# Performance work log

Measured on AMD Instinct MI355X. Metric: run time of the kernel, lower is better.

## Reference

```python
import jax, jax.numpy as jnp
import numpy as np
import math

D_PAIR = 64
N_HEADS = 4
D_HEAD = D_PAIR // N_HEADS


def setup_inputs() -> dict:
    key = jax.random.key(0)
    ks = jax.random.split(key, 9)
    B, L, D = 2, 256, D_PAIR
    s = 1.0 / math.sqrt(D)
    return {
        "z": jax.random.normal(ks[0], (B, L, L, D), dtype=jnp.float32),
        "ln_scale": jnp.ones((D,), jnp.float32),
        "ln_bias": jnp.zeros((D,), jnp.float32),
        "Wq": jax.random.normal(ks[1], (D, D), jnp.float32) * s,
        "Wk": jax.random.normal(ks[2], (D, D), jnp.float32) * s,
        "Wv": jax.random.normal(ks[3], (D, D), jnp.float32) * s,
        "Wg": jax.random.normal(ks[4], (D, D), jnp.float32) * s,
        "bg": jax.random.normal(ks[5], (D,), jnp.float32) * 0.02,
        "Wo": jax.random.normal(ks[6], (D, D), jnp.float32) * s,
        "bo": jax.random.normal(ks[7], (D,), jnp.float32) * 0.02,
    }


def _layernorm(x, scale, bias, eps=1e-5):
    mu = jnp.mean(x, axis=-1, keepdims=True)
    var = jnp.var(x, axis=-1, keepdims=True)
    return (x - mu) * jax.lax.rsqrt(var + eps) * scale + bias


def reference(z, ln_scale, ln_bias, Wq, Wk, Wv, Wg, bg, Wo, bo):
    B, L, _, D = z.shape
    H, Dh = N_HEADS, D_HEAD
    zn = _layernorm(z, ln_scale, ln_bias)
    # torch Linear(no bias): x @ W.T
    Q = (zn @ Wq.T).reshape(B, L, L, H, Dh)
    K = (zn @ Wk.T).reshape(B, L, L, H, Dh)
    V = (zn @ Wv.T).reshape(B, L, L, H, Dh)
    scale = 1.0 / math.sqrt(Dh)
    # row-wise attention: for each row l, attend over column index j
    attn = jnp.einsum("blihd,bljhd->blhij", Q, K) * scale  # [B,L,H,L,L]
    attn = jax.nn.softmax(attn, axis=-1)
    out = jnp.einsum("blhij,bljhd->blihd", attn, V).reshape(B, L, L, D)
    gate = jax.nn.sigmoid(zn @ Wg.T + bg)
    out = gate * out
    return out @ Wo.T + bo
```

## Files before the change

kernel.cpp:

```cpp
#include <hip/hip_runtime.h>
#include <hip/hip_bf16.h>
#include <math.h>


typedef __attribute__((ext_vector_type(4))) float f32x4;
typedef __attribute__((ext_vector_type(8))) short s16x8;

#define MFMA16(a, b, c) __builtin_amdgcn_mfma_f32_16x16x32_bf16((a), (b), (c), 0, 0, 0)

__device__ __forceinline__ float exp2a(float x) {
    float r;
    asm("v_exp_f32 %0, %1" : "=v"(r) : "v"(x));
    return r;
}
__device__ __forceinline__ float rcpa(float x) {
    float r;
    asm("v_rcp_f32 %0, %1" : "=v"(r) : "v"(x));
    return r;
}

__device__ __forceinline__ unsigned pk2(float a, float b) {
    union { __hip_bfloat162 h; unsigned u; } c;
    float2 t; t.x = a; t.y = b;
    c.h = __float22bfloat162_rn(t);
    return c.u;
}
__device__ __forceinline__ s16x8 cvt8(const float* p) {
    union { unsigned u[4]; s16x8 v; } r;
    r.u[0] = pk2(p[0], p[1]); r.u[1] = pk2(p[2], p[3]);
    r.u[2] = pk2(p[4], p[5]); r.u[3] = pk2(p[6], p[7]);
    return r.v;
}

static constexpr int WSLICE = 2560;
static constexpr int ZNL = 0;
static constexpr int KSH = 10240;
static constexpr int VT  = 14336;
static constexpr int LDS_EL = 18560;

__global__ __launch_bounds__(256, 3)
void ka_fused(const float* __restrict__ z, const float* __restrict__ ln_s,
              const float* __restrict__ ln_b, const float* __restrict__ Wq,
              const float* __restrict__ Wk, const float* __restrict__ Wv,
              const float* __restrict__ Wg, const float* __restrict__ bg,
              short* __restrict__ ws)
{
    __shared__ __align__(16) short lds[LDS_EL];
    const int tid = threadIdx.x, lane = tid & 63, w = tid >> 6;
    const int n16 = lane & 15, quad = lane >> 4;
    const bool qlo = (quad < 2);
    const int g = blockIdx.x, bl = g >> 2, h = g & 3;
    const size_t rowbase = (size_t)bl * (256 * 64);
    const int wsl = w * WSLICE;

    union { unsigned u[32]; s16x8 v8[8]; } row;
    {
        float zn[64];
        const float4* zp4 = (const float4*)(z + rowbase + (size_t)tid * 64);
        #pragma unroll
        for (int gq = 0; gq < 16; ++gq) {
            float4 v4 = zp4[gq];
            zn[gq * 4 + 0] = v4.x; zn[gq * 4 + 1] = v4.y;
            zn[gq * 4 + 2] = v4.z; zn[gq * 4 + 3] = v4.w;
        }
        float mu = 0.f;
        #pragma unroll
        for (int k = 0; k < 64; ++k) mu += zn[k];
        mu *= (1.f / 64.f);
        float va = 0.f;
        #pragma unroll
        for (int k = 0; k < 64; ++k) { float d = zn[k] - mu; va += d * d; }
        const float rs = rsqrtf(va * (1.f / 64.f) + 1e-5f);
        #pragma unroll
        for (int k = 0; k < 64; ++k) zn[k] = (zn[k] - mu) * rs * ln_s[k] + ln_b[k];
        #pragma unroll
        for (int k = 0; k < 32; ++k) row.u[k] = pk2(zn[2 * k], zn[2 * k + 1]);
    }

    auto store_row = [&](int slot) {
        #pragma unroll
        for (int gq = 0; gq < 8; ++gq)
            *(s16x8*)&lds[ZNL + wsl + slot * 1024 + (lane & 15) * 64
                          + ((gq ^ (lane & 7)) * 8)] = row.v8[gq];
    };

    s16x8 bq[2], bk[2], bv[2], bgf[2];
    #pragma unroll
    for (int ks = 0; ks < 2; ++ks) {
        size_t off = (size_t)(h * 16 + n16) * 64 + ks * 32 + quad * 8;
        bq[ks] = cvt8(Wq + off);  bk[ks] = cvt8(Wk + off);
        bv[ks] = cvt8(Wv + off);  bgf[ks] = cvt8(Wg + off);
    }
    const float4 bg4 = *(const float4*)(bg + h * 16 + quad * 4);
    constexpr float QS  = 0.25f;
    constexpr float L2E = 1.44269504088896340736f;

    float g4t[4][4];
    s16x8 qa[4];
    auto proj_tile = [&](int t, int s) {
        s16x8 zn0 = *(const s16x8*)&lds[ZNL + wsl + s * 1024 + n16 * 64
                                        + ((quad ^ (n16 & 7)) * 8)];
        s16x8 zn1 = *(const s16x8*)&lds[ZNL + wsl + s * 1024 + n16 * 64
                                        + (((4 + quad) ^ (n16 & 7)) * 8)];
        f32x4 aq = {}, ak = {}, av = {}, ag = {};
        aq = MFMA16(bq[0], zn0, aq);  aq = MFMA16(bq[1], zn1, aq);
        ak = MFMA16(bk[0], zn0, ak);  ak = MFMA16(bk[1], zn1, ak);
        ag = MFMA16(bgf[0], zn0, ag); ag = MFMA16(bgf[1], zn1, ag);
        av = MFMA16(zn0, bv[0], av);  av = MFMA16(zn1, bv[1], av);
        {
            uint2 p = {pk2(aq[0] * QS, aq[1] * QS), pk2(aq[2] * QS, aq[3] * QS)};
            *(uint2*)&lds[ZNL + wsl + 2048 + n16 * 16 + quad * 4] = p;
        }
        {
            uint2 p = {pk2(ak[0], ak[1]), pk2(ak[2], ak[3])};
            *(uint2*)&lds[KSH + (w * 64 + t * 16 + n16) * 16 + quad * 4] = p;
        }
        {
            uint2 p = {pk2(av[0], av[1]), pk2(av[2], av[3])};
            *(uint2*)&lds[VT + n16 * 264 + (w * 64 + t * 16 + quad * 4)] = p;
        }
        #pragma unroll
        for (int r = 0; r < 4; ++r)
            g4t[t][r] = rcpa(1.f + __expf(-(ag[r] + bg4[r])));
        s16x8 q = {};
        if (qlo) q = *(const s16x8*)&lds[ZNL + wsl + 2048 + n16 * 16 + quad * 8];
        qa[t] = q;
    };

    if (lane < 32) store_row(lane >> 4);
    proj_tile(0, 0);
    if (lane >= 32 && lane < 48) store_row(0);
    proj_tile(1, 1);
    if (lane >= 48) store_row(1);
    proj_tile(2, 0);
    proj_tile(3, 1);
    __syncthreads();

    f32x4 o4[4], lacc[4];
    #pragma unroll
    for (int qt = 0; qt < 4; ++qt) { o4[qt] = {}; lacc[qt] = {}; }
    s16x8 ones;
    {
        union { unsigned u[4]; s16x8 v; } c;
        c.u[0] = 0x3F803F80u; c.u[1] = 0x3F803F80u;
        c.u[2] = 0x3F803F80u; c.u[3] = 0x3F803F80u;
        ones = c.v;
    }
    const int sw = (n16 ^ (n16 >> 2)) & 3;
    for (int ch = 0; ch < 8; ++ch) {
        #pragma unroll
        for (int jtl = 0; jtl < 2; ++jtl) {
            int jt = ch * 2 + jtl;
            s16x8 kf = *(const s16x8*)&lds[KSH + (jt * 16 + n16) * 16 + quad * 8];
            const int po = (((jtl * 2 + (quad >> 1)) ^ sw) * 8) + (quad & 1) * 4;
            #pragma unroll
            for (int qt = 0; qt < 4; ++qt) {
                f32x4 zc = {};
                f32x4 s = MFMA16(kf, qa[qt], zc);
                float e0 = exp2a(s[0] * L2E), e1 = exp2a(s[1] * L2E);
                float e2 = exp2a(s[2] * L2E), e3 = exp2a(s[3] * L2E);
                uint2 p = {pk2(e0, e1), pk2(e2, e3)};
                *(uint2*)&lds[ZNL + wsl + qt * 640 + n16 * 40 + po] = p;
            }
        }
        s16x8 vf = *(const s16x8*)&lds[VT + n16 * 264 + ch * 32 + quad * 8];
        #pragma unroll
        for (int qt = 0; qt < 4; ++qt) {
            s16x8 pf = *(const s16x8*)&lds[ZNL + wsl + qt * 640 + n16 * 40
                                           + ((quad ^ sw) * 8)];
            o4[qt]   = MFMA16(vf, pf, o4[qt]);
            lacc[qt] = MFMA16(ones, pf, lacc[qt]);
        }
    }

    #pragma unroll
    for (int qt = 0; qt < 4; ++qt) {
        const float l = (lacc[qt][0] + lacc[qt][1]) * 0.5f;
        const float inv = rcpa(l);
        float g0 = g4t[qt][0] * o4[qt][0] * inv;
        float g1 = g4t[qt][1] * o4[qt][1] * inv;
        float g2 = g4t[qt][2] * o4[qt][2] * inv;
        float g3 = g4t[qt][3] * o4[qt][3] * inv;
        uint2 p = {pk2(g0, g1), pk2(g2, g3)};
        short* dst = ws + (((size_t)h * 512 + bl) * 256 + w * 64 + qt * 16 + n16) * 16
                     + quad * 4;
        *(uint2*)dst = p;
    }
}

__global__ __launch_bounds__(256, 4)
void k3_out(const short* __restrict__ ws, const float* __restrict__ Wo,
            const float* __restrict__ bo, float* __restrict__ out)
{
    const int tid = threadIdx.x, lane = tid & 63, w = tid >> 6;
    const int n16 = lane & 15, quad = lane >> 4;
    const short* GO = ws;
    const int bl = blockIdx.x >> 1, half = blockIdx.x & 1;
    const int rowloc = half * 128 + w * 32;

    s16x8 bfr[4][2];
    #pragma unroll
    for (int nt = 0; nt < 4; ++nt)
        #pragma unroll
        for (int ks = 0; ks < 2; ++ks)
            bfr[nt][ks] = cvt8(Wo + (size_t)(nt * 16 + n16) * 64 + ks * 32 + quad * 8);

    f32x4 acc[2][4] = {};
    #pragma unroll
    for (int mt = 0; mt < 2; ++mt) {
        #pragma unroll
        for (int c = 0; c < 2; ++c) {
            int hp = c * 2 + (quad >> 1);
            const short* ap = &GO[(((size_t)hp * 512 + bl) * 256 + rowloc + mt * 16 + n16) * 16
                                  + (quad & 1) * 8];
            s16x8 a = *(const s16x8*)ap;
            #pragma unroll
            for (int nt = 0; nt < 4; ++nt)
                acc[mt][nt] = MFMA16(bfr[nt][c], a, acc[mt][nt]);
        }
    }
    #pragma unroll
    for (int nt = 0; nt < 4; ++nt) {
        const float4 b4 = *(const float4*)(bo + nt * 16 + quad * 4);
        f32x4 b4v; b4v[0] = b4.x; b4v[1] = b4.y; b4v[2] = b4.z; b4v[3] = b4.w;
        #pragma unroll
        for (int mt = 0; mt < 2; ++mt) {
            f32x4 v = acc[mt][nt] + b4v;
            *(f32x4*)&out[((size_t)bl * 256 + rowloc + mt * 16 + n16) * 64
                          + nt * 16 + quad * 4] = v;
        }
    }
}

extern "C" void kernel_launch(void* const* d_in, const int* in_sizes, int n_in,
                              void* d_out, int out_size, void* d_ws, size_t ws_size,
                              hipStream_t stream) {
    const float* z  = (const float*)d_in[0];
    const float* ls = (const float*)d_in[1];
    const float* lb = (const float*)d_in[2];
    const float* Wq = (const float*)d_in[3];
    const float* Wk = (const float*)d_in[4];
    const float* Wv = (const float*)d_in[5];
    const float* Wg = (const float*)d_in[6];
    const float* bg = (const float*)d_in[7];
    const float* Wo = (const float*)d_in[8];
    const float* bo = (const float*)d_in[9];
    float* out = (float*)d_out;
    short* wsp = (short*)d_ws;

    hipLaunchKernelGGL(ka_fused, dim3(2048), dim3(256), 0, stream,
                       z, ls, lb, Wq, Wk, Wv, Wg, bg, wsp);
    hipLaunchKernelGGL(k3_out, dim3(1024), dim3(256), 0, stream, wsp, Wo, bo, out);
}
```

Before: 160.7 us.

## Keep softmax probabilities in registers using 16x16x16 bf16 MFMA layout

Switches the QK^T and PV MFMAs from the 16x16x32 to the 16x16x16 bf16 instruction, so the score accumulator layout matches the B-operand layout directly. This removes the LDS round-trip for probabilities (write then re-read with swizzle) and keeps Q in registers instead of staging it through LDS. It also shrinks the per-wave LDS slice and pads the K rows. In exchange it issues twice as many MFMA instructions, each with half the K depth, and carries an inline-asm fallback with fixed nops if the builtin is missing.

```diff
diff --git a/kernel.cpp b/kernel.cpp
--- a/kernel.cpp
+++ b/kernel.cpp
@@ -5,8 +5,25 @@
 
 typedef __attribute__((ext_vector_type(4))) float f32x4;
 typedef __attribute__((ext_vector_type(8))) short s16x8;
+typedef __attribute__((ext_vector_type(4))) short s16x4;
 
 #define MFMA16(a, b, c) __builtin_amdgcn_mfma_f32_16x16x32_bf16((a), (b), (c), 0, 0, 0)
+
+__device__ __forceinline__ f32x4 mfma16b(s16x4 a, s16x4 b, f32x4 c) {
+#if __has_builtin(__builtin_amdgcn_mfma_f32_16x16x16bf16_1k)
+    return __builtin_amdgcn_mfma_f32_16x16x16bf16_1k(a, b, c, 0, 0, 0);
+#elif __has_builtin(__builtin_amdgcn_mfma_f32_16x16x16_bf16)
+    return __builtin_amdgcn_mfma_f32_16x16x16_bf16(a, b, c, 0, 0, 0);
+#else
+    f32x4 d;
+    asm volatile("s_nop 1\n\t"
+                 "v_mfma_f32_16x16x16_bf16 %0, %1, %2, %3\n\t"
+                 "s_nop 7\n\t"
+                 "s_nop 7"
+                 : "=v"(d) : "v"(a), "v"(b), "v"(c));
+    return d;
+#endif
+}
 
 __device__ __forceinline__ float exp2a(float x) {
     float r;
@@ -32,11 +49,11 @@
     return r.v;
 }
 
-static constexpr int WSLICE = 2560;
+static constexpr int WSLICE = 2048;
 static constexpr int ZNL = 0;
-static constexpr int KSH = 10240;
-static constexpr int VT  = 14336;
-static constexpr int LDS_EL = 18560;
+static constexpr int KSH = 8192;
+static constexpr int VT  = 13312;
+static constexpr int LDS_EL = 17536;
 
 __global__ __launch_bounds__(256, 3)
 void ka_fused(const float* __restrict__ z, const float* __restrict__ ln_s,
@@ -48,7 +65,6 @@
     __shared__ __align__(16) short lds[LDS_EL];
     const int tid = threadIdx.x, lane = tid & 63, w = tid >> 6;
     const int n16 = lane & 15, quad = lane >> 4;
-    const bool qlo = (quad < 2);
     const int g = blockIdx.x, bl = g >> 2, h = g & 3;
     const size_t rowbase = (size_t)bl * (256 * 64);
     const int wsl = w * WSLICE;
@@ -96,7 +112,7 @@
     constexpr float L2E = 1.44269504088896340736f;
 
     float g4t[4][4];
-    s16x8 qa[4];
+    s16x4 qa4[4];
     auto proj_tile = [&](int t, int s) {
         s16x8 zn0 = *(const s16x8*)&lds[ZNL + wsl + s * 1024 + n16 * 64
                                         + ((quad ^ (n16 & 7)) * 8)];
@@ -108,12 +124,14 @@
         ag = MFMA16(bgf[0], zn0, ag); ag = MFMA16(bgf[1], zn1, ag);
         av = MFMA16(zn0, bv[0], av);  av = MFMA16(zn1, bv[1], av);
         {
-            uint2 p = {pk2(aq[0] * QS, aq[1] * QS), pk2(aq[2] * QS, aq[3] * QS)};
-            *(uint2*)&lds[ZNL + wsl + 2048 + n16 * 16 + quad * 4] = p;
+            union { unsigned u[2]; s16x4 v; } q;
+            q.u[0] = pk2(aq[0] * QS, aq[1] * QS);
+            q.u[1] = pk2(aq[2] * QS, aq[3] * QS);
+            qa4[t] = q.v;
         }
         {
             uint2 p = {pk2(ak[0], ak[1]), pk2(ak[2], ak[3])};
-            *(uint2*)&lds[KSH + (w * 64 + t * 16 + n16) * 16 + quad * 4] = p;
+            *(uint2*)&lds[KSH + (w * 64 + t * 16 + n16) * 20 + quad * 4] = p;
         }
         {
             uint2 p = {pk2(av[0], av[1]), pk2(av[2], av[3])};
@@ -122,9 +140,6 @@
         #pragma unroll
         for (int r = 0; r < 4; ++r)
             g4t[t][r] = rcpa(1.f + __expf(-(ag[r] + bg4[r])));
-        s16x8 q = {};
-        if (qlo) q = *(const s16x8*)&lds[ZNL + wsl + 2048 + n16 * 16 + quad * 8];
-        qa[t] = q;
     };
 
     if (lane < 32) store_row(lane >> 4);
@@ -139,37 +154,31 @@
     f32x4 o4[4], lacc[4];
     #pragma unroll
     for (int qt = 0; qt < 4; ++qt) { o4[qt] = {}; lacc[qt] = {}; }
-    s16x8 ones;
+    s16x4 ones4;
     {
-        union { unsigned u[4]; s16x8 v; } c;
+        union { unsigned u[2]; s16x4 v; } c;
         c.u[0] = 0x3F803F80u; c.u[1] = 0x3F803F80u;
-        c.u[2] = 0x3F803F80u; c.u[3] = 0x3F803F80u;
-        ones = c.v;
-    }
-    const int sw = (n16 ^ (n16 >> 2)) & 3;
+        ones4 = c.v;
+    }
+    const int kbase = KSH + n16 * 20 + quad * 4;
+    const int vbase = VT + n16 * 264 + quad * 4;
     for (int ch = 0; ch < 8; ++ch) {
         #pragma unroll
         for (int jtl = 0; jtl < 2; ++jtl) {
-            int jt = ch * 2 + jtl;
-            s16x8 kf = *(const s16x8*)&lds[KSH + (jt * 16 + n16) * 16 + quad * 8];
-            const int po = (((jtl * 2 + (quad >> 1)) ^ sw) * 8) + (quad & 1) * 4;
+            const int jt = ch * 2 + jtl;
+            s16x4 kf = *(const s16x4*)&lds[kbase + jt * 320];
+            s16x4 vf = *(const s16x4*)&lds[vbase + jt * 16];
             #pragma unroll
             for (int qt = 0; qt < 4; ++qt) {
                 f32x4 zc = {};
-                f32x4 s = MFMA16(kf, qa[qt], zc);
+                f32x4 s = mfma16b(kf, qa4[qt], zc);
                 float e0 = exp2a(s[0] * L2E), e1 = exp2a(s[1] * L2E);
                 float e2 = exp2a(s[2] * L2E), e3 = exp2a(s[3] * L2E);
-                uint2 p = {pk2(e0, e1), pk2(e2, e3)};
-                *(uint2*)&lds[ZNL + wsl + qt * 640 + n16 * 40 + po] = p;
+                union { unsigned u[2]; s16x4 v; } pb;
+                pb.u[0] = pk2(e0, e1); pb.u[1] = pk2(e2, e3);
+                o4[qt]   = mfma16b(vf, pb.v, o4[qt]);
+                lacc[qt] = mfma16b(ones4, pb.v, lacc[qt]);
             }
-        }
-        s16x8 vf = *(const s16x8*)&lds[VT + n16 * 264 + ch * 32 + quad * 8];
-        #pragma unroll
-        for (int qt = 0; qt < 4; ++qt) {
-            s16x8 pf = *(const s16x8*)&lds[ZNL + wsl + qt * 640 + n16 * 40
-                                           + ((quad ^ sw) * 8)];
-            o4[qt]   = MFMA16(vf, pf, o4[qt]);
-            lacc[qt] = MFMA16(ones, pf, lacc[qt]);
         }
     }
 
```

Result: faster. 155.1 us (-3.5%).
